# Kernel tuning notes

Measured on AMD Instinct MI355X. Metric: run time of the kernel, lower is better.

## Reference

```python
import jax, jax.numpy as jnp
import numpy as np

B, S, D, H = 2, 4096, 512, 8
DH = D // H
EPS = 1e-5


def setup_inputs() -> dict:
    key = jax.random.key(0)
    ks = jax.random.split(key, 8)
    s = 0.02
    return {
        "x": jax.random.normal(ks[0], (B, S, D), jnp.float32),
        "in_proj_w": jax.random.normal(ks[1], (3 * D, D), jnp.float32) * s,
        "in_proj_b": jnp.zeros((3 * D,), jnp.float32),
        "out_proj_w": jax.random.normal(ks[2], (D, D), jnp.float32) * s,
        "out_proj_b": jnp.zeros((D,), jnp.float32),
        "ln1_g": jnp.ones((D,), jnp.float32),
        "ln1_b": jnp.zeros((D,), jnp.float32),
        "ln2_g": jnp.ones((D,), jnp.float32),
        "ln2_b": jnp.zeros((D,), jnp.float32),
        "w1": jax.random.normal(ks[3], (D, D), jnp.float32) * s,
        "b1": jnp.zeros((D,), jnp.float32),
        "w2": jax.random.normal(ks[4], (D, D), jnp.float32) * s,
        "b2": jnp.zeros((D,), jnp.float32),
        "window": 256,
    }


def _layernorm(x, g, b):
    mu = jnp.mean(x, axis=-1, keepdims=True)
    var = jnp.mean(jnp.square(x - mu), axis=-1, keepdims=True)
    return (x - mu) * jax.lax.rsqrt(var + EPS) * g + b


def reference(x, in_proj_w, in_proj_b, out_proj_w, out_proj_b,
              ln1_g, ln1_b, ln2_g, ln2_b, w1, b1, w2, b2, window):
    b, s, d = x.shape
    # sliding-window mask: allowed iff |i - j| <= window
    idx = jnp.arange(s)
    allowed = jnp.abs(idx[:, None] - idx[None, :]) <= window  # [S,S]

    # fused QKV projection (torch MultiheadAttention layout: W [3D, D])
    qkv = x @ in_proj_w.T + in_proj_b  # [B,S,3D]
    q, k, v = jnp.split(qkv, 3, axis=-1)
    q = q.reshape(b, s, H, DH)
    k = k.reshape(b, s, H, DH)
    v = v.reshape(b, s, H, DH)

    scale = 1.0 / jnp.sqrt(jnp.float32(DH))
    scores = jnp.einsum("bqhd,bkhd->bhqk", q, k) * scale  # [B,H,S,S]
    scores = jnp.where(allowed[None, None], scores, -jnp.inf)
    attn = jax.nn.softmax(scores, axis=-1)
    ctx = jnp.einsum("bhqk,bkhd->bqhd", attn, v).reshape(b, s, d)
    attn_out = ctx @ out_proj_w.T + out_proj_b

    # residual + LayerNorm (dropout rate 0 -> identity)
    h = _layernorm(x + attn_out, ln1_g, ln1_b)
    mlp = jax.nn.relu(h @ w1.T + b1) @ w2.T + b2
    return _layernorm(h + mlp, ln2_g, ln2_b)
```

## Files before the change

kernel.cpp:

```cpp
#include <hip/hip_runtime.h>

typedef __bf16 bf16;
typedef __bf16 bf16x2 __attribute__((ext_vector_type(2)));
typedef __bf16 bf16x8 __attribute__((ext_vector_type(8)));
typedef float f32x4 __attribute__((ext_vector_type(4)));

#define S_LEN 4096
#define DMODEL 512
#define NHEAD 8
#define DHEAD 64
#define BATCH 2
#define M_ROWS (BATCH * S_LEN)
#define K_DIM 512
#define QKV_LD 1536

__device__ __forceinline__ void async16(void* lds, const void* g) {
  __builtin_amdgcn_global_load_lds(
      (const __attribute__((address_space(1))) unsigned int*)g,
      (__attribute__((address_space(3))) unsigned int*)lds, 16, 0, 0);
}

__global__ void detect_dtype(const unsigned int* __restrict__ x,
                             int* __restrict__ flag) {
  const int lane = threadIdx.x;
  int cnt = 0;
#pragma unroll
  for (int i = 0; i < 16; ++i) {
    const unsigned int w = x[lane * 16 + i];
    const unsigned int e = (w >> 7) & 0xFFu;
    cnt += (e >= 100u && e <= 140u) ? 1 : 0;
  }
#pragma unroll
  for (int off = 1; off < 64; off <<= 1) cnt += __shfl_xor(cnt, off);
  if (lane == 0) *flag = (cnt >= 700) ? 1 : 0;
}

__device__ __forceinline__ bf16x8 ld8(const void* p, size_t e, bool asF32) {
  if (asF32) {
    const float* q = (const float*)p + e;
    const float4 a = *(const float4*)q;
    const float4 b = *(const float4*)(q + 4);
    bf16x8 r;
    r[0] = (bf16)a.x; r[1] = (bf16)a.y; r[2] = (bf16)a.z; r[3] = (bf16)a.w;
    r[4] = (bf16)b.x; r[5] = (bf16)b.y; r[6] = (bf16)b.z; r[7] = (bf16)b.w;
    return r;
  }
  return *(const bf16x8*)((const bf16*)p + e);
}

__device__ __forceinline__ float ld1(const void* p, size_t e, bool asF32) {
  return asF32 ? ((const float*)p)[e] : (float)((const bf16*)p)[e];
}

__global__ __launch_bounds__(256) void cvt_all(const void* __restrict__ x,
                                               const void* __restrict__ s0,
                                               const void* __restrict__ s1,
                                               const void* __restrict__ s2,
                                               const void* __restrict__ s3,
                                               bf16* __restrict__ xb,
                                               bf16* __restrict__ warena,
                                               const int* __restrict__ flag) {
  const bool f32in = (*flag == 0);
  const int b = blockIdx.x;
  if (b < 2048) {
    const size_t idx = ((size_t)b * 256 + threadIdx.x) * 8;
    *(bf16x8*)(xb + idx) = ld8(x, idx, f32in);
    return;
  }
  const int wb = b - 2048;
  const void* s;
  size_t doff;
  int lb;
  if (wb < 384)      { s = s0; doff = 0;        lb = wb; }
  else if (wb < 512) { s = s1; doff = 786432;   lb = wb - 384; }
  else if (wb < 640) { s = s2; doff = 1048576;  lb = wb - 512; }
  else               { s = s3; doff = 1310720;  lb = wb - 640; }
  const size_t idx = (size_t)lb * 2048 + threadIdx.x * 8;
  *(bf16x8*)(warena + doff + idx) = ld8(s, idx, f32in);
}

template <int NMAT, int BN, bool RELU>
__global__ __launch_bounds__(256) void gemm_bt(const bf16* __restrict__ A,
                                               const bf16* __restrict__ W,
                                               const void* __restrict__ bias,
                                               bf16* __restrict__ C,
                                               const int* __restrict__ flag) {
  __shared__ __align__(16) bf16 As[128 * 64];
  __shared__ __align__(16) bf16 Ws[BN * 64];

  const bool f32in = (*flag == 0);

  const int t = threadIdx.x;
  const int lane = t & 63;
  const int wave = t >> 6;
  constexpr int MT = (BN == 128) ? 4 : 2;
  const int wm = (BN == 128) ? (wave >> 1) * 64 : wave * 32;
  const int wn = (BN == 128) ? (wave & 1) * 64 : 0;
  const int l16 = lane & 15;
  const int quad = lane >> 4;

  constexpr int NB = NMAT / BN;
  constexpr int MPX = (M_ROWS / 128) / 8;
  const int bid = blockIdx.x;
  const int xcd = bid & 7;
  const int r = bid >> 3;
  const int m0 = (xcd * MPX + r / NB) * 128;
  const int n0 = (r % NB) * BN;

  const int rr = lane >> 3;
  const int cb = (lane & 7) ^ rr;
  const int sw = l16 & 7;

  f32x4 acc[MT][4];
#pragma unroll
  for (int i = 0; i < MT; ++i)
#pragma unroll
    for (int j = 0; j < 4; ++j) acc[i][j] = (f32x4){0.f, 0.f, 0.f, 0.f};

  for (int kt = 0; kt < K_DIM; kt += 64) {
    __syncthreads();
#pragma unroll
    for (int i = 0; i < 4; ++i) {
      const int r0 = wave * 32 + i * 8;
      async16(&As[r0 * 64], &A[(size_t)(m0 + r0 + rr) * K_DIM + kt + cb * 8]);
    }
#pragma unroll
    for (int i = 0; i < BN / 32; ++i) {
      const int r0 = wave * (BN / 4) + i * 8;
      async16(&Ws[r0 * 64], &W[(size_t)(n0 + r0 + rr) * K_DIM + kt + cb * 8]);
    }
    __syncthreads();
#pragma unroll
    for (int ks = 0; ks < 2; ++ks) {
      bf16x8 af[MT], wf[4];
#pragma unroll
      for (int mt = 0; mt < MT; ++mt)
        af[mt] = *(const bf16x8*)&As[(wm + mt * 16 + l16) * 64 +
                                     (((ks * 4 + quad) ^ sw) * 8)];
#pragma unroll
      for (int nt = 0; nt < 4; ++nt)
        wf[nt] = *(const bf16x8*)&Ws[(wn + nt * 16 + l16) * 64 +
                                     (((ks * 4 + quad) ^ sw) * 8)];
#pragma unroll
      for (int mt = 0; mt < MT; ++mt)
#pragma unroll
        for (int nt = 0; nt < 4; ++nt)
          acc[mt][nt] = __builtin_amdgcn_mfma_f32_16x16x32_bf16(af[mt], wf[nt],
                                                                acc[mt][nt], 0, 0, 0);
    }
  }

#pragma unroll
  for (int nt = 0; nt < 4; ++nt) {
    const int n = n0 + wn + nt * 16 + l16;
    const float bv = ld1(bias, n, f32in);
#pragma unroll
    for (int mt = 0; mt < MT; ++mt) {
#pragma unroll
      for (int r4 = 0; r4 < 4; ++r4) {
        const int m = m0 + wm + mt * 16 + quad * 4 + r4;
        float v = acc[mt][nt][r4] + bv;
        if (RELU) v = fmaxf(v, 0.f);
        C[(size_t)m * NMAT + n] = (bf16)v;
      }
    }
  }
}

__global__ __launch_bounds__(256) void attn_fwd(const bf16* __restrict__ qkv,
                                                bf16* __restrict__ ctx,
                                                const int* __restrict__ wptr) {
  __shared__ __align__(16) bf16 Vt[2][64][72];
  __shared__ __align__(16) bf16 Pbuf[4][16][72];

  const int t = threadIdx.x;
  const int lane = t & 63;
  const int wave = t >> 6;
  const int l16 = lane & 15;
  const int quad = lane >> 4;

  const int bid = blockIdx.x;
  const int xcd = bid & 7;
  const int jj = bid >> 3;
  const int pair = xcd * 2 + (jj >> 6);
  const int qblk = jj & 63;
  const int h = pair & 7;
  const int b = pair >> 3;
  const int qbase = qblk * 64;
  int window = *wptr;
  if (window < 0) window = 0;
  if (window > S_LEN) window = S_LEN;
  const float scale = 0.125f;

  const int qrow = qbase + wave * 16 + l16;
  const bf16* qp = qkv + (size_t)(b * S_LEN + qrow) * QKV_LD + h * DHEAD;
  const bf16x8 qf0 = *(const bf16x8*)(qp + quad * 8);
  const bf16x8 qf1 = *(const bf16x8*)(qp + 32 + quad * 8);

  f32x4 o[4];
#pragma unroll
  for (int nt = 0; nt < 4; ++nt) o[nt] = (f32x4){0.f, 0.f, 0.f, 0.f};
  float lp[4] = {0.f, 0.f, 0.f, 0.f};

  int kstart = qbase - window;
  if (kstart < 0) kstart = 0;
  kstart &= ~63;
  int kend = qbase + 64 + window;
  if (kend > S_LEN) kend = S_LEN;
  const int niter = (kend - kstart + 63) >> 6;

  const int vk = (t & 31) * 2;
  const int vd = (t >> 5) * 8;
  const bf16* vbase = qkv + (size_t)(b * S_LEN) * QKV_LD + 2 * DMODEL + h * DHEAD + vd;
  const bf16* kbase = qkv + (size_t)(b * S_LEN) * QKV_LD + DMODEL + h * DHEAD;

  {
    const bf16* p = vbase + (size_t)(kstart + vk) * QKV_LD;
    const bf16x8 va = *(const bf16x8*)p;
    const bf16x8 vb = *(const bf16x8*)(p + QKV_LD);
#pragma unroll
    for (int j = 0; j < 8; ++j) {
      bf16x2 pr; pr[0] = va[j]; pr[1] = vb[j];
      *(bf16x2*)&Vt[0][vd + j][vk] = pr;
    }
  }

  for (int it = 0; it < niter; ++it) {
    const int kt = kstart + it * 64;
    const int cur = it & 1;
    __syncthreads();

    bf16x8 na, nb;
    const bool have_next = (it + 1 < niter);
    if (have_next) {
      const bf16* p = vbase + (size_t)(kt + 64 + vk) * QKV_LD;
      na = *(const bf16x8*)p;
      nb = *(const bf16x8*)(p + QKV_LD);
    }

    f32x4 s[4];
#pragma unroll
    for (int t4 = 0; t4 < 4; ++t4) s[t4] = (f32x4){0.f, 0.f, 0.f, 0.f};
#pragma unroll
    for (int t4 = 0; t4 < 4; ++t4) {
      const bf16* kp = kbase + (size_t)(kt + t4 * 16 + l16) * QKV_LD;
      const bf16x8 k0 = *(const bf16x8*)(kp + quad * 8);
      const bf16x8 k1 = *(const bf16x8*)(kp + 32 + quad * 8);
      s[t4] = __builtin_amdgcn_mfma_f32_16x16x32_bf16(qf0, k0, s[t4], 0, 0, 0);
      s[t4] = __builtin_amdgcn_mfma_f32_16x16x32_bf16(qf1, k1, s[t4], 0, 0, 0);
    }

#pragma unroll
    for (int r = 0; r < 4; ++r) {
      const int q = qbase + wave * 16 + quad * 4 + r;
      const int lo = q - window, hi = q + window;
      float psum = 0.f;
#pragma unroll
      for (int t4 = 0; t4 < 4; ++t4) {
        const int key = kt + t4 * 16 + l16;
        const float p = (key >= lo && key <= hi) ? __expf(s[t4][r] * scale) : 0.f;
        psum += p;
        Pbuf[wave][quad * 4 + r][t4 * 16 + l16] = (bf16)p;
      }
      lp[r] += psum;
    }

    const bf16x8 pf0 = *(const bf16x8*)&Pbuf[wave][l16][quad * 8];
    const bf16x8 pf1 = *(const bf16x8*)&Pbuf[wave][l16][32 + quad * 8];
#pragma unroll
    for (int nt = 0; nt < 4; ++nt) {
      const bf16x8 v0 = *(const bf16x8*)&Vt[cur][nt * 16 + l16][quad * 8];
      const bf16x8 v1 = *(const bf16x8*)&Vt[cur][nt * 16 + l16][32 + quad * 8];
      o[nt] = __builtin_amdgcn_mfma_f32_16x16x32_bf16(pf0, v0, o[nt], 0, 0, 0);
      o[nt] = __builtin_amdgcn_mfma_f32_16x16x32_bf16(pf1, v1, o[nt], 0, 0, 0);
    }

    if (have_next) {
#pragma unroll
      for (int j = 0; j < 8; ++j) {
        bf16x2 pr; pr[0] = na[j]; pr[1] = nb[j];
        *(bf16x2*)&Vt[cur ^ 1][vd + j][vk] = pr;
      }
    }
  }

#pragma unroll
  for (int r = 0; r < 4; ++r) {
#pragma unroll
    for (int off = 1; off < 16; off <<= 1) lp[r] += __shfl_xor(lp[r], off);
    const float inv = (lp[r] > 0.f) ? (1.0f / lp[r]) : 0.f;
    const int q = qbase + wave * 16 + quad * 4 + r;
#pragma unroll
    for (int nt = 0; nt < 4; ++nt) {
      ctx[(size_t)(b * S_LEN + q) * DMODEL + h * DHEAD + nt * 16 + l16] =
          (bf16)(o[nt][r] * inv);
    }
  }
}

template <bool A_RAW, bool OUT_RAW>
__global__ __launch_bounds__(256) void ln_fused(const void* __restrict__ a,
                                                const bf16* __restrict__ bres,
                                                const void* __restrict__ g,
                                                const void* __restrict__ be,
                                                void* __restrict__ out,
                                                const int* __restrict__ flag) {
  const bool f32in = (*flag == 0);
  const int row = blockIdx.x * 4 + (threadIdx.x >> 6);
  const int lane = threadIdx.x & 63;
  const size_t base = (size_t)row * DMODEL + lane * 8;
  const bf16x8 va = ld8(a, base, A_RAW && f32in);
  const bf16x8 vb = *(const bf16x8*)(bres + base);
  float v[8], s = 0.f, s2 = 0.f;
#pragma unroll
  for (int j = 0; j < 8; ++j) {
    v[j] = (float)va[j] + (float)vb[j];
    s += v[j];
    s2 += v[j] * v[j];
  }
#pragma unroll
  for (int off = 1; off < 64; off <<= 1) {
    s += __shfl_xor(s, off);
    s2 += __shfl_xor(s2, off);
  }
  const float mean = s * (1.0f / DMODEL);
  float var = s2 * (1.0f / DMODEL) - mean * mean;
  if (var < 0.f) var = 0.f;
  const float rstd = rsqrtf(var + 1e-5f);
  const bf16x8 gv = ld8(g, lane * 8, f32in);
  const bf16x8 bev = ld8(be, lane * 8, f32in);
  float ov[8];
#pragma unroll
  for (int j = 0; j < 8; ++j)
    ov[j] = (v[j] - mean) * rstd * (float)gv[j] + (float)bev[j];
  if (OUT_RAW && f32in) {
    float4 o0 = {ov[0], ov[1], ov[2], ov[3]};
    float4 o1 = {ov[4], ov[5], ov[6], ov[7]};
    *(float4*)((float*)out + base) = o0;
    *(float4*)((float*)out + base + 4) = o1;
  } else {
    bf16x8 ob;
#pragma unroll
    for (int j = 0; j < 8; ++j) ob[j] = (bf16)ov[j];
    *(bf16x8*)((bf16*)out + base) = ob;
  }
}

extern "C" void kernel_launch(void* const* d_in, const int* in_sizes, int n_in,
                              void* d_out, int out_size, void* d_ws, size_t ws_size,
                              hipStream_t stream) {
  const void* x          = d_in[0];
  const void* in_proj_w  = d_in[1];
  const void* in_proj_b  = d_in[2];
  const void* out_proj_w = d_in[3];
  const void* out_proj_b = d_in[4];
  const void* ln1_g      = d_in[5];
  const void* ln1_b      = d_in[6];
  const void* ln2_g      = d_in[7];
  const void* ln2_b      = d_in[8];
  const void* w1         = d_in[9];
  const void* b1         = d_in[10];
  const void* w2         = d_in[11];
  const void* b2         = d_in[12];
  const int*  wptr       = (const int*)d_in[13];

  char* ws = (char*)d_ws;
  int* flag = (int*)ws;
  bf16* warena = (bf16*)(ws + 256);
  bf16* wq = warena;
  bf16* wo = warena + 786432;
  bf16* w1b = warena + 1048576;
  bf16* w2b = warena + 1310720;
  char* big = ws + 256 + 3145728;
  bf16* qkv      = (bf16*)big;
  bf16* h        = (bf16*)big;
  bf16* a1       = (bf16*)(big + 8388608);
  bf16* attn_out = (bf16*)(big + 16777216);
  bf16* mlp      = attn_out;
  bf16* xb       = (bf16*)d_out;
  bf16* ctx      = (bf16*)d_out;

  detect_dtype<<<1, 64, 0, stream>>>((const unsigned int*)x, flag);
  cvt_all<<<2816, 256, 0, stream>>>(x, in_proj_w, out_proj_w, w1, w2, xb, warena, flag);
  gemm_bt<QKV_LD, 128, false><<<768, 256, 0, stream>>>(
      xb, wq, in_proj_b, qkv, flag);
  attn_fwd<<<dim3(BATCH * NHEAD * (S_LEN / 64)), 256, 0, stream>>>(qkv, ctx, wptr);
  gemm_bt<DMODEL, 64, false><<<512, 256, 0, stream>>>(
      ctx, wo, out_proj_b, attn_out, flag);
  ln_fused<true, false><<<dim3(M_ROWS / 4), 256, 0, stream>>>(
      x, attn_out, ln1_g, ln1_b, h, flag);
  gemm_bt<DMODEL, 64, true><<<512, 256, 0, stream>>>(
      h, w1b, b1, a1, flag);
  gemm_bt<DMODEL, 64, false><<<512, 256, 0, stream>>>(
      a1, w2b, b2, mlp, flag);
  ln_fused<false, true><<<dim3(M_ROWS / 4), 256, 0, stream>>>(
      h, mlp, ln2_g, ln2_b, d_out, flag);
}
```

Before: 221.4 us.

## Prefetch K tiles into registers one iteration ahead in attention loop

New measurement: 267.0 us. +20.6%, slower.

```diff
diff --git a/kernel.cpp b/kernel.cpp
--- a/kernel.cpp
+++ b/kernel.cpp
@@ -167,9 +167,9 @@
   }
 }
 
-__global__ __launch_bounds__(256) void attn_fwd(const bf16* __restrict__ qkv,
-                                                bf16* __restrict__ ctx,
-                                                const int* __restrict__ wptr) {
+__global__ __launch_bounds__(256, 4) void attn_fwd(const bf16* __restrict__ qkv,
+                                                   bf16* __restrict__ ctx,
+                                                   const int* __restrict__ wptr) {
   __shared__ __align__(16) bf16 Vt[2][64][72];
   __shared__ __align__(16) bf16 Pbuf[4][16][72];
 
@@ -190,7 +190,7 @@
   int window = *wptr;
   if (window < 0) window = 0;
   if (window > S_LEN) window = S_LEN;
-  const float scale = 0.125f;
+  const float sc_log2e = 0.125f * 1.44269504f;
 
   const int qrow = qbase + wave * 16 + l16;
   const bf16* qp = qkv + (size_t)(b * S_LEN + qrow) * QKV_LD + h * DHEAD;
@@ -225,7 +225,16 @@
     }
   }
 
-  for (int it = 0; it < niter; ++it) {
+  auto loadK = [&](bf16x8 (&kr)[8], int kt) {
+#pragma unroll
+    for (int t4 = 0; t4 < 4; ++t4) {
+      const bf16* kp = kbase + (size_t)(kt + t4 * 16 + l16) * QKV_LD;
+      kr[t4 * 2]     = *(const bf16x8*)(kp + quad * 8);
+      kr[t4 * 2 + 1] = *(const bf16x8*)(kp + 32 + quad * 8);
+    }
+  };
+
+  auto body = [&](int it, bf16x8 (&kc)[8], bf16x8 (&kn)[8]) {
     const int kt = kstart + it * 64;
     const int cur = it & 1;
     __syncthreads();
@@ -236,6 +245,7 @@
       const bf16* p = vbase + (size_t)(kt + 64 + vk) * QKV_LD;
       na = *(const bf16x8*)p;
       nb = *(const bf16x8*)(p + QKV_LD);
+      loadK(kn, kt + 64);
     }
 
     f32x4 s[4];
@@ -243,11 +253,8 @@
     for (int t4 = 0; t4 < 4; ++t4) s[t4] = (f32x4){0.f, 0.f, 0.f, 0.f};
 #pragma unroll
     for (int t4 = 0; t4 < 4; ++t4) {
-      const bf16* kp = kbase + (size_t)(kt + t4 * 16 + l16) * QKV_LD;
-      const bf16x8 k0 = *(const bf16x8*)(kp + quad * 8);
-      const bf16x8 k1 = *(const bf16x8*)(kp + 32 + quad * 8);
-      s[t4] = __builtin_amdgcn_mfma_f32_16x16x32_bf16(qf0, k0, s[t4], 0, 0, 0);
-      s[t4] = __builtin_amdgcn_mfma_f32_16x16x32_bf16(qf1, k1, s[t4], 0, 0, 0);
+      s[t4] = __builtin_amdgcn_mfma_f32_16x16x32_bf16(qf0, kc[t4 * 2], s[t4], 0, 0, 0);
+      s[t4] = __builtin_amdgcn_mfma_f32_16x16x32_bf16(qf1, kc[t4 * 2 + 1], s[t4], 0, 0, 0);
     }
 
 #pragma unroll
@@ -258,7 +265,9 @@
 #pragma unroll
       for (int t4 = 0; t4 < 4; ++t4) {
         const int key = kt + t4 * 16 + l16;
-        const float p = (key >= lo && key <= hi) ? __expf(s[t4][r] * scale) : 0.f;
+        const float p = (key >= lo && key <= hi)
+                            ? __builtin_amdgcn_exp2f(s[t4][r] * sc_log2e)
+                            : 0.f;
         psum += p;
         Pbuf[wave][quad * 4 + r][t4 * 16 + l16] = (bf16)p;
       }
@@ -282,7 +291,16 @@
         *(bf16x2*)&Vt[cur ^ 1][vd + j][vk] = pr;
       }
     }
-  }
+  };
+
+  bf16x8 ka[8], kb[8];
+  loadK(ka, kstart);
+  int it = 0;
+  for (; it + 2 <= niter; it += 2) {
+    body(it, ka, kb);
+    body(it + 1, kb, ka);
+  }
+  if (it < niter) body(it, ka, kb);
 
 #pragma unroll
   for (int r = 0; r < 4; ++r) {
```
